# Kernel tuning notes

Hardware: AMD Instinct MI355X
Metric: run time of the kernel (lower is better)

## Reference

```python
import jax, jax.numpy as jnp
import numpy as np

B, N, F, K, FILT = 256, 256, 128, 4, 256  # batch mols, max_atom, Fin, Chebyshev order, nb_filter
EPS = float(np.spacing(np.float32(0)))    # matches np.spacing(0) in original degree normalization
D2_FLOOR = 1e-12                          # numerical floor for sqrt of pairwise sq-dist


def setup_inputs() -> dict:
    key = jax.random.key(0)
    ks = jax.random.split(key, 6)
    x = jax.random.normal(ks[0], (B, N, F), dtype=jnp.float32)
    lap_in = 0.1 * jax.random.normal(ks[1], (B, N, N), dtype=jnp.float32)  # input per-mol Laplacian
    n_atoms = jax.random.randint(ks[2], (B,), 64, N + 1, dtype=jnp.int32)  # ragged mol sizes
    r1 = float(np.sqrt(6.0 / (F + F)))
    M_L = jax.random.uniform(ks[3], (F, F), jnp.float32, -r1, r1)          # Mahalanobis metric
    r2 = float(np.sqrt(6.0 / (F * K + FILT)))
    weight = jax.random.uniform(ks[4], (F * K, FILT), jnp.float32, -r2, r2)
    bias = jnp.zeros((FILT,), jnp.float32)
    return {"x": x, "lap_in": lap_in, "n_atoms": n_atoms, "M_L": M_L, "weight": weight, "bias": bias}


def reference(x, lap_in, n_atoms, M_L, weight, bias):
    # mask[b,n] = 1 for real atoms, 0 for padding (replaces per-mol tf.slice + pad)
    mask = (jnp.arange(N)[None, :] < n_atoms[:, None]).astype(x.dtype)       # [B,N]
    x = x * mask[..., None]

    # ---- learned Laplacian: Mahalanobis RBF affinity + sym degree normalization ----
    xw = jnp.einsum('bnf,fg->bng', x, M_L)                                   # x @ M_L
    sq = jnp.sum(xw * xw, axis=-1)                                           # [B,N]
    d2 = sq[:, :, None] + sq[:, None, :] - 2.0 * jnp.einsum('bif,bjf->bij', xw, xw)
    eye = jnp.eye(N, dtype=x.dtype)
    off = mask[:, :, None] * mask[:, None, :] * (1.0 - eye)                  # valid off-diag pairs
    d2_safe = jnp.where(off > 0, jnp.maximum(d2, D2_FLOOR), 1.0)
    W = jnp.exp(-jnp.sqrt(d2_safe)) * off                                    # W[i,j]=exp(-dist), diag 0
    deg = jnp.sum(W, axis=1) + EPS                                           # W symmetric: axis0==axis1
    dinv = jnp.where(mask > 0, 1.0 / jnp.sqrt(deg), 0.0)                     # D^{-1/2} (0 on padding)
    # L = I - D^{-1/2} W D^{-1/2} (intended math of the original py_func)
    L_learn = eye[None] * mask[:, :, None] - dinv[:, :, None] * W * dinv[:, None, :]
    L = L_learn + lap_in * (mask[:, :, None] * mask[:, None, :])             # L + sliced input LL

    # ---- Chebyshev recurrence: x0=x, x1=Lx, xk = 2 L x_{k-1} - x_{k-2} ----
    x0 = x
    x1 = jnp.einsum('bij,bjf->bif', L, x0)
    xs = [x0, x1]
    for _ in range(2, K):
        x2 = 2.0 * jnp.einsum('bij,bjf->bif', L, x1) - x0
        xs.append(x2)
        x0, x1 = x1, x2
    # stack -> [B,N,F,K] then flatten (f,k) row-major, matching reshape([K,M,F])->transpose([1,2,0])->reshape([M,K*F])
    xc = jnp.stack(xs, axis=-1).reshape(B, N, F * K)

    out = jnp.einsum('bnd,do->bno', xc, weight) + bias                       # [B,N,FILT]
    out = jax.nn.relu(out * mask[..., None])                                 # pad-to-max_atom + relu
    return out, L_learn
```

## Files before the change

### kernel.cpp

```cpp
#include <hip/hip_runtime.h>
#include <math.h>

typedef __bf16 bf16;
typedef __bf16 bf16x8 __attribute__((ext_vector_type(8)));
typedef __bf16 bf16x4 __attribute__((ext_vector_type(4)));
typedef float f32x4 __attribute__((ext_vector_type(4)));

constexpr int cB = 256, cN = 256, cF = 128, cO = 256;
constexpr int BN = cB * cN;
constexpr float D2_FLOOR = 1e-12f;
constexpr float EPS_F = 1.401298464324817e-45f;

constexpr size_t OFF_XC  = 0;
constexpr size_t OFF_XW  = OFF_XC + (size_t)BN * 512 * 2;
constexpr size_t OFF_X0T = OFF_XW + (size_t)BN * 128 * 2;
constexpr size_t OFF_LB  = OFF_X0T + (size_t)cB * cF * cN * 2;
constexpr size_t OFF_WB  = OFF_LB + (size_t)cB * cN * cN * 2;
constexpr size_t OFF_WT  = OFF_WB + (size_t)cB * cN * cN * 2;
constexpr size_t OFF_MT  = OFF_WT + 512 * 256 * 2;
constexpr size_t OFF_SQ  = OFF_MT + 128 * 128 * 2;
constexpr size_t OFF_DEG = OFF_SQ + (size_t)BN * 4;

__device__ __forceinline__ bf16x8 gfrag(const bf16* __restrict__ p, int ld,
                                        int lane, int k0) {
  return *(const bf16x8*)(p + (size_t)(lane & 15) * ld + k0 + 8 * (lane >> 4));
}

__device__ __forceinline__ f32x4 mfma(bf16x8 a, bf16x8 b, f32x4 c) {
  return __builtin_amdgcn_mfma_f32_16x16x32_bf16(a, b, c, 0, 0, 0);
}

__device__ __forceinline__ void gll16(const void* g, void* l) {
  __builtin_amdgcn_global_load_lds((const __attribute__((address_space(1))) void*)g,
                                   (__attribute__((address_space(3))) void*)l, 16, 0, 0);
}

__global__ __launch_bounds__(256) void k_prep(const float* __restrict__ x,
                                              const int* __restrict__ na_p,
                                              bf16* __restrict__ xc,
                                              bf16* __restrict__ x0T) {
  __shared__ __align__(16) bf16 T[64][132];
  int b = blockIdx.x >> 2, i0 = (blockIdx.x & 3) * 64;
  int tid = threadIdx.x;
  int na = na_p[b];
#pragma unroll
  for (int it = 0; it < 8; ++it) {
    int ir = it * 8 + (tid >> 5);
    int f0 = (tid & 31) * 4;
    int i = i0 + ir;
    float m = (i < na) ? 1.f : 0.f;
    float4 v = *(const float4*)(x + ((size_t)b * cN + i) * cF + f0);
    bf16x4 pk = {(bf16)(v.x * m), (bf16)(v.y * m), (bf16)(v.z * m), (bf16)(v.w * m)};
    *(bf16x4*)(xc + ((size_t)b * cN + i) * 512 + f0) = pk;
    *(bf16x4*)(&T[ir][f0]) = pk;
  }
  __syncthreads();
  int f = tid >> 1, half = tid & 1;
  bf16* od = x0T + ((size_t)b * cF + f) * cN + i0 + half * 32;
#pragma unroll
  for (int c = 0; c < 32; c += 4) {
    int ii = half * 32 + c;
    bf16x4 pk = {T[ii][f], T[ii + 1][f], T[ii + 2][f], T[ii + 3][f]};
    *(bf16x4*)(od + c) = pk;
  }
}

__global__ __launch_bounds__(256) void k_wt(const float* __restrict__ wgt,
                                            const float* __restrict__ ML,
                                            bf16* __restrict__ Wt,
                                            bf16* __restrict__ MT) {
  int id = blockIdx.x * 256 + threadIdx.x;
  if (id < 512 * 256) {
    int o = id >> 9, d = id & 511;
    int k = d >> 7, f = d & 127;
    Wt[id] = (bf16)wgt[(f * 4 + k) * 256 + o];
  } else {
    int id2 = id - 512 * 256;
    if (id2 < 128 * 128) {
      int g = id2 >> 7, f = id2 & 127;
      MT[id2] = (bf16)ML[f * 128 + g];
    }
  }
}

__global__ __launch_bounds__(256, 4) void k_xw2(const bf16* __restrict__ xc,
                                                const bf16* __restrict__ MT,
                                                bf16* __restrict__ xw,
                                                float* __restrict__ sq) {
  __shared__ float sqb[64];
  int tid = threadIdx.x, wid = tid >> 6, lane = tid & 63;
  int r0 = blockIdx.x * 64;
  const bf16* A = xc + (size_t)r0 * 512;
  const bf16* Bg = MT + (size_t)(wid * 32) * 128;
  f32x4 acc[4][2] = {};
#pragma unroll
  for (int ks = 0; ks < 4; ++ks) {
    int k0 = ks * 32;
    bf16x8 b0 = gfrag(Bg, 128, lane, k0);
    bf16x8 b1 = gfrag(Bg + 16 * 128, 128, lane, k0);
#pragma unroll
    for (int mf = 0; mf < 4; ++mf) {
      bf16x8 a = gfrag(A + (size_t)mf * 16 * 512, 512, lane, k0);
      acc[mf][0] = mfma(a, b0, acc[mf][0]);
      acc[mf][1] = mfma(a, b1, acc[mf][1]);
    }
  }
  if (tid < 64) sqb[tid] = 0.f;
  __syncthreads();
  int hi = lane >> 4, il = lane & 15;
#pragma unroll
  for (int mf = 0; mf < 4; ++mf) {
#pragma unroll
    for (int r = 0; r < 4; ++r) {
      int row = r0 + mf * 16 + 4 * hi + r;
      float s = 0.f;
#pragma unroll
      for (int nf = 0; nf < 2; ++nf) {
        bf16 v = (bf16)acc[mf][nf][r];
        xw[(size_t)row * cF + wid * 32 + nf * 16 + il] = v;
        float f = (float)v;
        s = fmaf(f, f, s);
      }
      s += __shfl_xor(s, 1); s += __shfl_xor(s, 2);
      s += __shfl_xor(s, 4); s += __shfl_xor(s, 8);
      if (il == 0) atomicAdd(&sqb[mf * 16 + 4 * hi + r], s);
    }
  }
  __syncthreads();
  if (tid < 64) sq[r0 + tid] = sqb[tid];
}

__global__ __launch_bounds__(256, 4) void k_gram2(const bf16* __restrict__ xw,
                                                  const float* __restrict__ sq,
                                                  const int* __restrict__ na_p,
                                                  bf16* __restrict__ Wb16,
                                                  float* __restrict__ deg) {
  __shared__ float lsq[256];
  int bx = blockIdx.x;
  int b = bx >> 2, i0 = ((bx >> 1) & 1) * 128, j0 = (bx & 1) * 128;
  int tid = threadIdx.x, wid = tid >> 6, lane = tid & 63;
  int wm = wid >> 1, wn = wid & 1;
  lsq[tid] = sq[b * cN + tid];
  const bf16* X = xw + (size_t)b * cN * cF;
  const bf16* Ag = X + (size_t)(i0 + wm * 64) * cF;
  const bf16* Bg = X + (size_t)(j0 + wn * 64) * cF;
  f32x4 acc[4][4] = {};
#pragma unroll
  for (int ks = 0; ks < 4; ++ks) {
    int k0 = ks * 32;
    bf16x8 bb[4];
#pragma unroll
    for (int nf = 0; nf < 4; ++nf) bb[nf] = gfrag(Bg + (size_t)nf * 16 * cF, cF, lane, k0);
#pragma unroll
    for (int mf = 0; mf < 4; ++mf) {
      bf16x8 a = gfrag(Ag + (size_t)mf * 16 * cF, cF, lane, k0);
#pragma unroll
      for (int nf = 0; nf < 4; ++nf) acc[mf][nf] = mfma(a, bb[nf], acc[mf][nf]);
    }
  }
  __syncthreads();
  int na = na_p[b];
  int hi = lane >> 4, il = lane & 15;
#pragma unroll
  for (int mf = 0; mf < 4; ++mf) {
#pragma unroll
    for (int r = 0; r < 4; ++r) {
      int i = i0 + wm * 64 + mf * 16 + 4 * hi + r;
      float sqi = lsq[i];
      bool mi = i < na;
      float rs = 0.f;
#pragma unroll
      for (int nf = 0; nf < 4; ++nf) {
        int j = j0 + wn * 64 + nf * 16 + il;
        float w = 0.f;
        if (mi && j < na && i != j) {
          float d2 = fmaxf(sqi + lsq[j] - 2.f * acc[mf][nf][r], D2_FLOOR);
          w = __expf(-sqrtf(d2));
        }
        Wb16[((size_t)b * cN + i) * cN + j] = (bf16)w;
        rs += w;
      }
      rs += __shfl_xor(rs, 1); rs += __shfl_xor(rs, 2);
      rs += __shfl_xor(rs, 4); rs += __shfl_xor(rs, 8);
      if (il == 0) atomicAdd(&deg[b * cN + i], rs);
    }
  }
}

__global__ __launch_bounds__(256) void k_Lassm(const bf16* __restrict__ Wb16,
                                               const float* __restrict__ deg,
                                               const float* __restrict__ lap,
                                               const int* __restrict__ na_p,
                                               bf16* __restrict__ Lb,
                                               float* __restrict__ llearn) {
  int tid = threadIdx.x;
  size_t e = ((size_t)blockIdx.x * 256 + tid) * 8;
  int b = (int)(e >> 16);
  int na = na_p[b];
  __shared__ float dinvl[256];
  dinvl[tid] = (tid < na) ? 1.f / sqrtf(deg[b * cN + tid] + EPS_F) : 0.f;
  __syncthreads();
  int j = (int)(e & 255);
  int i = (int)((e >> 8) & 255);
  bf16x8 w8 = *(const bf16x8*)(Wb16 + e);
  float4 lp0 = *(const float4*)(lap + e);
  float4 lp1 = *(const float4*)(lap + e + 4);
  float di = dinvl[i];
  float mi = (i < na) ? 1.f : 0.f;
  float4 ll0, ll1;
  bf16x8 lo;
#pragma unroll
  for (int c = 0; c < 8; ++c) {
    int jj = j + c;
    float v = -di * (float)w8[c] * dinvl[jj];
    if (i == jj && i < na) v += 1.f;
    float lpv = (c < 4) ? (&lp0.x)[c] : (&lp1.x)[c - 4];
    if (c < 4) (&ll0.x)[c] = v; else (&ll1.x)[c - 4] = v;
    float mj = (jj < na) ? 1.f : 0.f;
    lo[c] = (bf16)(v + lpv * mi * mj);
  }
  *(float4*)(llearn + e) = ll0;
  *(float4*)(llearn + e + 4) = ll1;
  *(bf16x8*)(Lb + e) = lo;
}

__device__ __forceinline__ void cheb_step(const bf16* __restrict__ Lm,
                                          const char* Bsrc, const char* Ppp,
                                          char* Odst, bf16* __restrict__ xcm,
                                          int kcol, int wid, int lane, bool haspp,
                                          bool wlds) {
  int hi = lane >> 4, il = lane & 15;
  int i0w = wid * 32;
  f32x4 acc[2][8] = {};
#pragma unroll
  for (int ks = 0; ks < 8; ++ks) {
    int k0 = ks * 32;
    bf16x8 a0 = gfrag(Lm + (size_t)i0w * cN, cN, lane, k0);
    bf16x8 a1 = gfrag(Lm + (size_t)(i0w + 16) * cN, cN, lane, k0);
#pragma unroll
    for (int nf = 0; nf < 8; ++nf) {
      int f = nf * 16 + il;
      const char* p = Bsrc + f * 512 + ((64 * ks + 16 * hi) ^ ((il & 7) << 4));
      bf16x8 bb = *(const bf16x8*)p;
      acc[0][nf] = mfma(a0, bb, acc[0][nf]);
      acc[1][nf] = mfma(a1, bb, acc[1][nf]);
    }
  }
#pragma unroll
  for (int mf = 0; mf < 2; ++mf) {
    int ib = i0w + mf * 16 + 4 * hi;
#pragma unroll
    for (int nf = 0; nf < 8; ++nf) {
      int f = nf * 16 + il;
      int cb = (2 * ib) ^ ((il & 7) << 4);
      bf16x4 o;
      if (haspp) {
        bf16x4 pp = *(const bf16x4*)(Ppp + f * 512 + cb);
#pragma unroll
        for (int r = 0; r < 4; ++r) o[r] = (bf16)(2.f * acc[mf][nf][r] - (float)pp[r]);
      } else {
#pragma unroll
        for (int r = 0; r < 4; ++r) o[r] = (bf16)acc[mf][nf][r];
      }
      if (wlds) *(bf16x4*)(Odst + f * 512 + cb) = o;
#pragma unroll
      for (int r = 0; r < 4; ++r)
        xcm[(size_t)(ib + r) * 512 + kcol + f] = o[r];
    }
  }
}

__global__ __launch_bounds__(512, 1) void k_cheb_f(const bf16* __restrict__ x0T,
                                                   const bf16* __restrict__ Lb,
                                                   bf16* __restrict__ xc) {
  __shared__ __align__(16) char XB[2][65536];
  int b = blockIdx.x;
  int tid = threadIdx.x, wid = tid >> 6, lane = tid & 63;
  const bf16* Lm = Lb + (size_t)b * cN * cN;
  bf16* xcm = xc + (size_t)b * cN * 512;
  const char* src = (const char*)(x0T + (size_t)b * cF * cN);
#pragma unroll
  for (int it = 0; it < 8; ++it) {
    int beta = it * 8192 + tid * 16;
    int f = beta >> 9, c = beta & 511;
    gll16(src + f * 512 + (c ^ ((f & 7) << 4)), XB[0] + beta);
  }
  __syncthreads();
  cheb_step(Lm, XB[0], nullptr, XB[1], xcm, 128, wid, lane, false, true);
  __syncthreads();
  cheb_step(Lm, XB[1], XB[0], XB[0], xcm, 256, wid, lane, true, true);
  __syncthreads();
  cheb_step(Lm, XB[0], XB[1], nullptr, xcm, 384, wid, lane, true, false);
}

__global__ __launch_bounds__(256, 4) void k_out2(const bf16* __restrict__ xc,
                                                 const bf16* __restrict__ Wt,
                                                 const float* __restrict__ bias,
                                                 const int* __restrict__ na_p,
                                                 float* __restrict__ out) {
  int tid = threadIdx.x, wid = tid >> 6, lane = tid & 63;
  int r0 = blockIdx.x * 64;
  const bf16* A = xc + (size_t)r0 * 512;
  const bf16* Bg = Wt + (size_t)(wid * 64) * 512;
  f32x4 acc[4][4] = {};
#pragma unroll 4
  for (int ks = 0; ks < 16; ++ks) {
    int k0 = ks * 32;
    bf16x8 bb[4];
#pragma unroll
    for (int nf = 0; nf < 4; ++nf) bb[nf] = gfrag(Bg + (size_t)nf * 16 * 512, 512, lane, k0);
#pragma unroll
    for (int mf = 0; mf < 4; ++mf) {
      bf16x8 a = gfrag(A + (size_t)mf * 16 * 512, 512, lane, k0);
#pragma unroll
      for (int nf = 0; nf < 4; ++nf) acc[mf][nf] = mfma(a, bb[nf], acc[mf][nf]);
    }
  }
  int na = na_p[r0 >> 8];
  int hi = lane >> 4, il = lane & 15;
#pragma unroll
  for (int nf = 0; nf < 4; ++nf) {
    int o = wid * 64 + nf * 16 + il;
    float bo = bias[o];
#pragma unroll
    for (int mf = 0; mf < 4; ++mf) {
#pragma unroll
      for (int r = 0; r < 4; ++r) {
        int row = r0 + mf * 16 + 4 * hi + r;
        float m = ((row & 255) < na) ? 1.f : 0.f;
        out[(size_t)row * cO + o] = fmaxf((acc[mf][nf][r] + bo) * m, 0.f);
      }
    }
  }
}

extern "C" void kernel_launch(void* const* d_in, const int* in_sizes, int n_in,
                              void* d_out, int out_size, void* d_ws, size_t ws_size,
                              hipStream_t stream) {
  const float* x    = (const float*)d_in[0];
  const float* lap  = (const float*)d_in[1];
  const int*   na   = (const int*)d_in[2];
  const float* M_L  = (const float*)d_in[3];
  const float* wgt  = (const float*)d_in[4];
  const float* bias = (const float*)d_in[5];

  float* out    = (float*)d_out;
  float* llearn = out + (size_t)BN * cO;

  char* ws = (char*)d_ws;
  bf16*  xc  = (bf16*)(ws + OFF_XC);
  bf16*  xw  = (bf16*)(ws + OFF_XW);
  bf16*  x0T = (bf16*)(ws + OFF_X0T);
  bf16*  Lb  = (bf16*)(ws + OFF_LB);
  bf16*  Wb  = (bf16*)(ws + OFF_WB);
  bf16*  Wt  = (bf16*)(ws + OFF_WT);
  bf16*  MT  = (bf16*)(ws + OFF_MT);
  float* sqb = (float*)(ws + OFF_SQ);
  float* deg = (float*)(ws + OFF_DEG);

  hipMemsetAsync(deg, 0, (size_t)BN * 4, stream);
  k_prep<<<dim3(1024), 256, 0, stream>>>(x, na, xc, x0T);
  k_wt<<<dim3(576), 256, 0, stream>>>(wgt, M_L, Wt, MT);
  k_xw2<<<dim3(1024), 256, 0, stream>>>(xc, MT, xw, sqb);
  k_gram2<<<dim3(1024), 256, 0, stream>>>(xw, sqb, na, Wb, deg);
  k_Lassm<<<dim3(8192), 256, 0, stream>>>(Wb, deg, lap, na, Lb, llearn);
  k_cheb_f<<<dim3(cB), 512, 0, stream>>>(x0T, Lb, xc);
  k_out2<<<dim3(1024), 256, 0, stream>>>(xc, Wt, bias, na, out);
}
```

Before: 391.1 us.

## Fuse xw projection with Gram kernel and Chebyshev with output GEMM

Merges the x@M_L projection and pairwise RBF Gram computation into one kernel per half-molecule that keeps xw and squared norms in LDS. This removes the xw/sq global round trip, the deg memset and the atomics. It also fuses the Chebyshev recurrence with the output weight GEMM, accumulating each Chebyshev slice's contribution in registers, so the 512-wide xc intermediate is never written to global memory. The cost is recomputing xw for both row halves, a large register footprint, and only 256 blocks for the fused output GEMM, which lowers parallelism.

```diff
diff --git a/kernel.cpp b/kernel.cpp
--- a/kernel.cpp
+++ b/kernel.cpp
@@ -11,15 +11,13 @@
 constexpr float D2_FLOOR = 1e-12f;
 constexpr float EPS_F = 1.401298464324817e-45f;
 
-constexpr size_t OFF_XC  = 0;
-constexpr size_t OFF_XW  = OFF_XC + (size_t)BN * 512 * 2;
-constexpr size_t OFF_X0T = OFF_XW + (size_t)BN * 128 * 2;
+constexpr size_t OFF_X0  = 0;
+constexpr size_t OFF_X0T = OFF_X0 + (size_t)BN * 128 * 2;
 constexpr size_t OFF_LB  = OFF_X0T + (size_t)cB * cF * cN * 2;
 constexpr size_t OFF_WB  = OFF_LB + (size_t)cB * cN * cN * 2;
 constexpr size_t OFF_WT  = OFF_WB + (size_t)cB * cN * cN * 2;
 constexpr size_t OFF_MT  = OFF_WT + 512 * 256 * 2;
-constexpr size_t OFF_SQ  = OFF_MT + 128 * 128 * 2;
-constexpr size_t OFF_DEG = OFF_SQ + (size_t)BN * 4;
+constexpr size_t OFF_DEG = OFF_MT + 128 * 128 * 2;
 
 __device__ __forceinline__ bf16x8 gfrag(const bf16* __restrict__ p, int ld,
                                         int lane, int k0) {
@@ -37,7 +35,7 @@
 
 __global__ __launch_bounds__(256) void k_prep(const float* __restrict__ x,
                                               const int* __restrict__ na_p,
-                                              bf16* __restrict__ xc,
+                                              bf16* __restrict__ X0,
                                               bf16* __restrict__ x0T) {
   __shared__ __align__(16) bf16 T[64][132];
   int b = blockIdx.x >> 2, i0 = (blockIdx.x & 3) * 64;
@@ -51,7 +49,7 @@
     float m = (i < na) ? 1.f : 0.f;
     float4 v = *(const float4*)(x + ((size_t)b * cN + i) * cF + f0);
     bf16x4 pk = {(bf16)(v.x * m), (bf16)(v.y * m), (bf16)(v.z * m), (bf16)(v.w * m)};
-    *(bf16x4*)(xc + ((size_t)b * cN + i) * 512 + f0) = pk;
+    *(bf16x4*)(X0 + ((size_t)b * cN + i) * cF + f0) = pk;
     *(bf16x4*)(&T[ir][f0]) = pk;
   }
   __syncthreads();
@@ -83,107 +81,88 @@
   }
 }
 
-__global__ __launch_bounds__(256, 4) void k_xw2(const bf16* __restrict__ xc,
-                                                const bf16* __restrict__ MT,
-                                                bf16* __restrict__ xw,
-                                                float* __restrict__ sq) {
-  __shared__ float sqb[64];
+__global__ __launch_bounds__(512, 2) void k_xwgram(const bf16* __restrict__ X0,
+                                                   const bf16* __restrict__ MT,
+                                                   const int* __restrict__ na_p,
+                                                   bf16* __restrict__ Wb16,
+                                                   float* __restrict__ deg) {
+  __shared__ __align__(16) char XW[65536];
+  __shared__ float lsq[256];
+  int bx = blockIdx.x;
+  int b = bx >> 1, h = bx & 1;
   int tid = threadIdx.x, wid = tid >> 6, lane = tid & 63;
-  int r0 = blockIdx.x * 64;
-  const bf16* A = xc + (size_t)r0 * 512;
-  const bf16* Bg = MT + (size_t)(wid * 32) * 128;
-  f32x4 acc[4][2] = {};
+  int hi = lane >> 4, il = lane & 15;
+
+  const bf16* A = X0 + ((size_t)b * cN + wid * 32) * cF;
+  f32x4 acc[2][8] = {};
 #pragma unroll
   for (int ks = 0; ks < 4; ++ks) {
     int k0 = ks * 32;
-    bf16x8 b0 = gfrag(Bg, 128, lane, k0);
-    bf16x8 b1 = gfrag(Bg + 16 * 128, 128, lane, k0);
-#pragma unroll
-    for (int mf = 0; mf < 4; ++mf) {
-      bf16x8 a = gfrag(A + (size_t)mf * 16 * 512, 512, lane, k0);
-      acc[mf][0] = mfma(a, b0, acc[mf][0]);
-      acc[mf][1] = mfma(a, b1, acc[mf][1]);
-    }
-  }
-  if (tid < 64) sqb[tid] = 0.f;
-  __syncthreads();
-  int hi = lane >> 4, il = lane & 15;
-#pragma unroll
-  for (int mf = 0; mf < 4; ++mf) {
+    bf16x8 a0 = gfrag(A, cF, lane, k0);
+    bf16x8 a1 = gfrag(A + 16 * cF, cF, lane, k0);
+#pragma unroll
+    for (int gt = 0; gt < 8; ++gt) {
+      bf16x8 bb = gfrag(MT + (size_t)gt * 16 * 128, 128, lane, k0);
+      acc[0][gt] = mfma(a0, bb, acc[0][gt]);
+      acc[1][gt] = mfma(a1, bb, acc[1][gt]);
+    }
+  }
+#pragma unroll
+  for (int nt = 0; nt < 2; ++nt) {
 #pragma unroll
     for (int r = 0; r < 4; ++r) {
-      int row = r0 + mf * 16 + 4 * hi + r;
+      int n = 32 * wid + 16 * nt + 4 * hi + r;
+      int swz = (n & 7) << 4;
       float s = 0.f;
 #pragma unroll
-      for (int nf = 0; nf < 2; ++nf) {
-        bf16 v = (bf16)acc[mf][nf][r];
-        xw[(size_t)row * cF + wid * 32 + nf * 16 + il] = v;
+      for (int gt = 0; gt < 8; ++gt) {
+        bf16 v = (bf16)acc[nt][gt][r];
+        *(bf16*)(XW + n * 256 + ((2 * (16 * gt + il)) ^ swz)) = v;
         float f = (float)v;
         s = fmaf(f, f, s);
       }
       s += __shfl_xor(s, 1); s += __shfl_xor(s, 2);
       s += __shfl_xor(s, 4); s += __shfl_xor(s, 8);
-      if (il == 0) atomicAdd(&sqb[mf * 16 + 4 * hi + r], s);
-    }
-  }
-  __syncthreads();
-  if (tid < 64) sq[r0 + tid] = sqb[tid];
-}
-
-__global__ __launch_bounds__(256, 4) void k_gram2(const bf16* __restrict__ xw,
-                                                  const float* __restrict__ sq,
-                                                  const int* __restrict__ na_p,
-                                                  bf16* __restrict__ Wb16,
-                                                  float* __restrict__ deg) {
-  __shared__ float lsq[256];
-  int bx = blockIdx.x;
-  int b = bx >> 2, i0 = ((bx >> 1) & 1) * 128, j0 = (bx & 1) * 128;
-  int tid = threadIdx.x, wid = tid >> 6, lane = tid & 63;
-  int wm = wid >> 1, wn = wid & 1;
-  lsq[tid] = sq[b * cN + tid];
-  const bf16* X = xw + (size_t)b * cN * cF;
-  const bf16* Ag = X + (size_t)(i0 + wm * 64) * cF;
-  const bf16* Bg = X + (size_t)(j0 + wn * 64) * cF;
-  f32x4 acc[4][4] = {};
+      if (il == 0) lsq[n] = s;
+    }
+  }
+  __syncthreads();
+
+  int ibase = h * 128 + 16 * wid;
+  int ia = ibase + il;
+  f32x4 g2[16] = {};
 #pragma unroll
   for (int ks = 0; ks < 4; ++ks) {
-    int k0 = ks * 32;
-    bf16x8 bb[4];
-#pragma unroll
-    for (int nf = 0; nf < 4; ++nf) bb[nf] = gfrag(Bg + (size_t)nf * 16 * cF, cF, lane, k0);
-#pragma unroll
-    for (int mf = 0; mf < 4; ++mf) {
-      bf16x8 a = gfrag(Ag + (size_t)mf * 16 * cF, cF, lane, k0);
-#pragma unroll
-      for (int nf = 0; nf < 4; ++nf) acc[mf][nf] = mfma(a, bb[nf], acc[mf][nf]);
-    }
-  }
-  __syncthreads();
+    int cb = 64 * ks + 16 * hi;
+    bf16x8 af = *(const bf16x8*)(XW + ia * 256 + (cb ^ ((ia & 7) << 4)));
+#pragma unroll
+    for (int jt = 0; jt < 16; ++jt) {
+      int j = 16 * jt + il;
+      bf16x8 bf_ = *(const bf16x8*)(XW + j * 256 + (cb ^ ((j & 7) << 4)));
+      g2[jt] = mfma(af, bf_, g2[jt]);
+    }
+  }
   int na = na_p[b];
-  int hi = lane >> 4, il = lane & 15;
-#pragma unroll
-  for (int mf = 0; mf < 4; ++mf) {
-#pragma unroll
-    for (int r = 0; r < 4; ++r) {
-      int i = i0 + wm * 64 + mf * 16 + 4 * hi + r;
-      float sqi = lsq[i];
-      bool mi = i < na;
-      float rs = 0.f;
-#pragma unroll
-      for (int nf = 0; nf < 4; ++nf) {
-        int j = j0 + wn * 64 + nf * 16 + il;
-        float w = 0.f;
-        if (mi && j < na && i != j) {
-          float d2 = fmaxf(sqi + lsq[j] - 2.f * acc[mf][nf][r], D2_FLOOR);
-          w = __expf(-sqrtf(d2));
-        }
-        Wb16[((size_t)b * cN + i) * cN + j] = (bf16)w;
-        rs += w;
+#pragma unroll
+  for (int r = 0; r < 4; ++r) {
+    int i = ibase + 4 * hi + r;
+    float sqi = lsq[i];
+    bool mi = i < na;
+    float rs = 0.f;
+#pragma unroll
+    for (int jt = 0; jt < 16; ++jt) {
+      int j = 16 * jt + il;
+      float w = 0.f;
+      if (mi && j < na && i != j) {
+        float d2 = fmaxf(sqi + lsq[j] - 2.f * g2[jt][r], D2_FLOOR);
+        w = __expf(-sqrtf(d2));
       }
-      rs += __shfl_xor(rs, 1); rs += __shfl_xor(rs, 2);
-      rs += __shfl_xor(rs, 4); rs += __shfl_xor(rs, 8);
-      if (il == 0) atomicAdd(&deg[b * cN + i], rs);
-    }
+      Wb16[((size_t)b * cN + i) * cN + j] = (bf16)w;
+      rs += w;
+    }
+    rs += __shfl_xor(rs, 1); rs += __shfl_xor(rs, 2);
+    rs += __shfl_xor(rs, 4); rs += __shfl_xor(rs, 8);
+    if (il == 0) deg[b * cN + i] = rs;
   }
 }
 
@@ -224,11 +203,9 @@
   *(bf16x8*)(Lb + e) = lo;
 }
 
-__device__ __forceinline__ void cheb_step(const bf16* __restrict__ Lm,
+__device__ __forceinline__ void cheb_pass(const bf16* __restrict__ Lm,
                                           const char* Bsrc, const char* Ppp,
-                                          char* Odst, bf16* __restrict__ xcm,
-                                          int kcol, int wid, int lane, bool haspp,
-                                          bool wlds) {
+                                          char* Odst, int wid, int lane, bool haspp) {
   int hi = lane >> 4, il = lane & 15;
   int i0w = wid * 32;
   f32x4 acc[2][8] = {};
@@ -262,23 +239,26 @@
 #pragma unroll
         for (int r = 0; r < 4; ++r) o[r] = (bf16)acc[mf][nf][r];
       }
-      if (wlds) *(bf16x4*)(Odst + f * 512 + cb) = o;
-#pragma unroll
-      for (int r = 0; r < 4; ++r)
-        xcm[(size_t)(ib + r) * 512 + kcol + f] = o[r];
-    }
-  }
-}
-
-__global__ __launch_bounds__(512, 1) void k_cheb_f(const bf16* __restrict__ x0T,
-                                                   const bf16* __restrict__ Lb,
-                                                   bf16* __restrict__ xc) {
+      *(bf16x4*)(Odst + f * 512 + cb) = o;
+    }
+  }
+}
+
+__global__ __launch_bounds__(512) void k_chebout(const bf16* __restrict__ x0T,
+                                                 const bf16* __restrict__ Lb,
+                                                 const bf16* __restrict__ Wt,
+                                                 const float* __restrict__ bias,
+                                                 const int* __restrict__ na_p,
+                                                 float* __restrict__ out) {
   __shared__ __align__(16) char XB[2][65536];
   int b = blockIdx.x;
   int tid = threadIdx.x, wid = tid >> 6, lane = tid & 63;
+  int hi = lane >> 4, il = lane & 15;
   const bf16* Lm = Lb + (size_t)b * cN * cN;
-  bf16* xcm = xc + (size_t)b * cN * 512;
   const char* src = (const char*)(x0T + (size_t)b * cF * cN);
+
+  f32x4 oacc[2][16] = {};
+
 #pragma unroll
   for (int it = 0; it < 8; ++it) {
     int beta = it * 8192 + tid * 16;
@@ -286,49 +266,55 @@
     gll16(src + f * 512 + (c ^ ((f & 7) << 4)), XB[0] + beta);
   }
   __syncthreads();
-  cheb_step(Lm, XB[0], nullptr, XB[1], xcm, 128, wid, lane, false, true);
-  __syncthreads();
-  cheb_step(Lm, XB[1], XB[0], XB[0], xcm, 256, wid, lane, true, true);
-  __syncthreads();
-  cheb_step(Lm, XB[0], XB[1], nullptr, xcm, 384, wid, lane, true, false);
-}
-
-__global__ __launch_bounds__(256, 4) void k_out2(const bf16* __restrict__ xc,
-                                                 const bf16* __restrict__ Wt,
-                                                 const float* __restrict__ bias,
-                                                 const int* __restrict__ na_p,
-                                                 float* __restrict__ out) {
-  int tid = threadIdx.x, wid = tid >> 6, lane = tid & 63;
-  int r0 = blockIdx.x * 64;
-  const bf16* A = xc + (size_t)r0 * 512;
-  const bf16* Bg = Wt + (size_t)(wid * 64) * 512;
-  f32x4 acc[4][4] = {};
-#pragma unroll 4
-  for (int ks = 0; ks < 16; ++ks) {
-    int k0 = ks * 32;
-    bf16x8 bb[4];
-#pragma unroll
-    for (int nf = 0; nf < 4; ++nf) bb[nf] = gfrag(Bg + (size_t)nf * 16 * 512, 512, lane, k0);
-#pragma unroll
-    for (int mf = 0; mf < 4; ++mf) {
-      bf16x8 a = gfrag(A + (size_t)mf * 16 * 512, 512, lane, k0);
-#pragma unroll
-      for (int nf = 0; nf < 4; ++nf) acc[mf][nf] = mfma(a, bb[nf], acc[mf][nf]);
-    }
-  }
-  int na = na_p[r0 >> 8];
-  int hi = lane >> 4, il = lane & 15;
-#pragma unroll
-  for (int nf = 0; nf < 4; ++nf) {
-    int o = wid * 64 + nf * 16 + il;
+
+#define SLICE(Bsrc, kst)                                                         \
+  {                                                                              \
+    const char* sb_ = (Bsrc);                                                    \
+    _Pragma("unroll")                                                            \
+    for (int ftp = 0; ftp < 4; ++ftp) {                                          \
+      bf16x8 av[2];                                                              \
+      _Pragma("unroll")                                                          \
+      for (int nt = 0; nt < 2; ++nt) {                                           \
+        int i_ = wid * 32 + nt * 16 + il;                                        \
+        _Pragma("unroll")                                                        \
+        for (int j = 0; j < 8; ++j) {                                            \
+          int f_ = 32 * ftp + 8 * hi + j;                                        \
+          av[nt][j] = *(const bf16*)(sb_ + f_ * 512 + ((2 * i_) ^ (j << 4)));    \
+        }                                                                        \
+      }                                                                          \
+      _Pragma("unroll")                                                          \
+      for (int ot = 0; ot < 16; ++ot) {                                          \
+        bf16x8 bb = gfrag(Wt + (size_t)(16 * ot) * 512, 512, lane,               \
+                          (kst) * 128 + 32 * ftp);                               \
+        oacc[0][ot] = mfma(av[0], bb, oacc[0][ot]);                              \
+        oacc[1][ot] = mfma(av[1], bb, oacc[1][ot]);                              \
+      }                                                                          \
+    }                                                                            \
+  }
+
+  SLICE(XB[0], 0);
+  cheb_pass(Lm, XB[0], nullptr, XB[1], wid, lane, false);
+  SLICE(XB[1], 1);
+  __syncthreads();
+  cheb_pass(Lm, XB[1], XB[0], XB[0], wid, lane, true);
+  SLICE(XB[0], 2);
+  __syncthreads();
+  cheb_pass(Lm, XB[0], XB[1], XB[1], wid, lane, true);
+  SLICE(XB[1], 3);
+#undef SLICE
+
+  int na = na_p[b];
+#pragma unroll
+  for (int ot = 0; ot < 16; ++ot) {
+    int o = 16 * ot + il;
     float bo = bias[o];
 #pragma unroll
-    for (int mf = 0; mf < 4; ++mf) {
+    for (int nt = 0; nt < 2; ++nt) {
 #pragma unroll
       for (int r = 0; r < 4; ++r) {
-        int row = r0 + mf * 16 + 4 * hi + r;
-        float m = ((row & 255) < na) ? 1.f : 0.f;
-        out[(size_t)row * cO + o] = fmaxf((acc[mf][nf][r] + bo) * m, 0.f);
+        int n = wid * 32 + nt * 16 + 4 * hi + r;
+        float m = (n < na) ? 1.f : 0.f;
+        out[((size_t)b * cN + n) * cO + o] = fmaxf((oacc[nt][ot][r] + bo) * m, 0.f);
       }
     }
   }
@@ -348,22 +334,17 @@
   float* llearn = out + (size_t)BN * cO;
 
   char* ws = (char*)d_ws;
-  bf16*  xc  = (bf16*)(ws + OFF_XC);
-  bf16*  xw  = (bf16*)(ws + OFF_XW);
+  bf16*  X0  = (bf16*)(ws + OFF_X0);
   bf16*  x0T = (bf16*)(ws + OFF_X0T);
   bf16*  Lb  = (bf16*)(ws + OFF_LB);
   bf16*  Wb  = (bf16*)(ws + OFF_WB);
   bf16*  Wt  = (bf16*)(ws + OFF_WT);
   bf16*  MT  = (bf16*)(ws + OFF_MT);
-  float* sqb = (float*)(ws + OFF_SQ);
   float* deg = (float*)(ws + OFF_DEG);
 
-  hipMemsetAsync(deg, 0, (size_t)BN * 4, stream);
-  k_prep<<<dim3(1024), 256, 0, stream>>>(x, na, xc, x0T);
+  k_prep<<<dim3(1024), 256, 0, stream>>>(x, na, X0, x0T);
   k_wt<<<dim3(576), 256, 0, stream>>>(wgt, M_L, Wt, MT);
-  k_xw2<<<dim3(1024), 256, 0, stream>>>(xc, MT, xw, sqb);
-  k_gram2<<<dim3(1024), 256, 0, stream>>>(xw, sqb, na, Wb, deg);
+  k_xwgram<<<dim3(512), 512, 0, stream>>>(X0, MT, na, Wb, deg);
   k_Lassm<<<dim3(8192), 256, 0, stream>>>(Wb, deg, lap, na, Lb, llearn);
-  k_cheb_f<<<dim3(cB), 512, 0, stream>>>(x0T, Lb, xc);
-  k_out2<<<dim3(1024), 256, 0, stream>>>(xc, Wt, bias, na, out);
-}
+  k_chebout<<<dim3(cB), 512, 0, stream>>>(x0T, Lb, Wt, bias, na, out);
+}
```

Measured after the change: 408.1 us. 4.3% more time.
